# Optimization experiments

Measured on AMD Instinct MI355X. Metric: run time of the kernel, lower is better.

## Reference

```python
import jax, jax.numpy as jnp
import numpy as np

B, S, D_IN, D_OUT = 2, 2048, 4096, 4096
NUM_HEADS, NUM_KV_GROUPS = 32, 8
HEAD_DIM = D_OUT // NUM_HEADS        # 128
GROUP_SIZE = NUM_HEADS // NUM_KV_GROUPS  # 4
ROPE_BASE = 10000.0


def _rope_tables(seq_len, head_dim, base):
    inv_freq = 1.0 / (base ** (jnp.arange(0, head_dim, 2, dtype=jnp.float32) / head_dim))
    pos = jnp.arange(seq_len, dtype=jnp.float32)
    angles = pos[:, None] * inv_freq[None, :]          # (S, hd/2)
    angles = jnp.concatenate([angles, angles], axis=-1)  # (S, hd)
    return jnp.cos(angles), jnp.sin(angles)


def _apply_rope(x, cos, sin):
    # x: (B, H, S, hd)
    hd = x.shape[-1]
    x1, x2 = x[..., : hd // 2], x[..., hd // 2 :]
    rotated = jnp.concatenate([-x2, x1], axis=-1)
    return x * cos[None, None, :, :] + rotated * sin[None, None, :, :]


def setup_inputs() -> dict:
    key = jax.random.key(0)
    k1, k2, k3, k4, k5 = jax.random.split(key, 5)
    s = 0.02
    return {
        "x": jax.random.normal(k1, (B, S, D_IN), jnp.float32),
        "Wq": jax.random.normal(k2, (D_OUT, D_IN), jnp.float32) * s,
        "Wk": jax.random.normal(k3, (NUM_KV_GROUPS * HEAD_DIM, D_IN), jnp.float32) * s,
        "Wv": jax.random.normal(k4, (NUM_KV_GROUPS * HEAD_DIM, D_IN), jnp.float32) * s,
        "Wo": jax.random.normal(k5, (D_OUT, D_OUT), jnp.float32) * s,
    }


def reference(x, Wq, Wk, Wv, Wo):
    b, s, _ = x.shape
    cos, sin = _rope_tables(s, HEAD_DIM, ROPE_BASE)

    # Projections (torch Linear: y = x @ W.T), reshape to (B, H, S, hd)
    q = (x @ Wq.T).reshape(b, s, NUM_HEADS, HEAD_DIM).transpose(0, 2, 1, 3)
    k = (x @ Wk.T).reshape(b, s, NUM_KV_GROUPS, HEAD_DIM).transpose(0, 2, 1, 3)
    v = (x @ Wv.T).reshape(b, s, NUM_KV_GROUPS, HEAD_DIM).transpose(0, 2, 1, 3)

    q = _apply_rope(q, cos, sin)
    k = _apply_rope(k, cos, sin)

    # repeat_interleave KV heads to match query heads
    k = jnp.repeat(k, GROUP_SIZE, axis=1)
    v = jnp.repeat(v, GROUP_SIZE, axis=1)

    scores = jnp.einsum("bhqd,bhkd->bhqk", q, k) / jnp.sqrt(jnp.float32(HEAD_DIM))
    causal = jnp.tril(jnp.ones((s, s), dtype=bool))
    scores = jnp.where(causal[None, None], scores, jnp.finfo(scores.dtype).min)
    attn = jax.nn.softmax(scores, axis=-1)

    ctx = jnp.einsum("bhqk,bhkd->bhqd", attn, v)  # (B, H, S, hd)
    ctx = ctx.transpose(0, 2, 1, 3).reshape(b, s, D_OUT)
    return ctx @ Wo.T
```

## Files before the change

### kernel.cpp

```cpp
#include <hip/hip_runtime.h>


typedef float f32x4 __attribute__((ext_vector_type(4)));
typedef short s16x8 __attribute__((ext_vector_type(8)));

union U8 { s16x8 v; unsigned int u[4]; };

__device__ __forceinline__ unsigned short f32_to_bf16(float f) {
    unsigned int u = __float_as_uint(f);
    u += 0x7fffu + ((u >> 16) & 1u);
    return (unsigned short)(u >> 16);
}
__device__ __forceinline__ float bf16_to_f32(unsigned short h) {
    return __uint_as_float(((unsigned int)h) << 16);
}
__device__ __forceinline__ unsigned int cvt_pk_bf16(float a, float b) {
    unsigned int r;
    asm("v_cvt_pk_bf16_f32 %0, %1, %2" : "=v"(r) : "v"(a), "v"(b));
    return r;
}
__device__ __forceinline__ void async16(const unsigned short* g, unsigned short* l) {
    __builtin_amdgcn_global_load_lds(
        (const __attribute__((address_space(1))) unsigned int*)g,
        (__attribute__((address_space(3))) unsigned int*)l, 16, 0, 0);
}

__global__ __launch_bounds__(256) void cast_f32_bf16(
    const float* __restrict__ in, unsigned short* __restrict__ out, int n4)
{
    int idx = blockIdx.x * 256 + threadIdx.x;
    if (idx >= n4) return;
    float4 v = ((const float4*)in)[idx];
    ushort4 o;
    o.x = f32_to_bf16(v.x); o.y = f32_to_bf16(v.y);
    o.z = f32_to_bf16(v.z); o.w = f32_to_bf16(v.w);
    ((ushort4*)out)[idx] = o;
}

template<int WRITE_F32>
__global__ __launch_bounds__(256) void gemm_bt(
    const unsigned short* __restrict__ A,
    const unsigned short* __restrict__ B,
    void* __restrict__ Cout, int M, int N, int K)
{
    __shared__ __attribute__((aligned(16))) unsigned short sA[2][128*32];
    __shared__ __attribute__((aligned(16))) unsigned short sB[2][128*32];
    const int tid  = threadIdx.x;
    const int lane = tid & 63;
    const int wv   = tid >> 6;
    const int wm   = (wv >> 1) * 64;
    const int wn   = (wv & 1) * 64;
    const int quad = lane >> 4;
    const int lr   = lane & 15;
    const int m0 = blockIdx.y * 128;
    const int n0 = blockIdx.x * 128;

    auto stage = [&](int kt, int bi) {
        const int k0 = kt << 5;
        #pragma unroll
        for (int p = 0; p < 2; ++p) {
            int e  = (p*256 + tid) * 8;
            int r  = e >> 5;
            int cc = (e & 31) >> 3;
            int gc = (cc ^ ((r >> 1) & 3)) * 8;
            async16(&A[(size_t)(m0 + r)*K + k0 + gc], &sA[bi][e]);
            async16(&B[(size_t)(n0 + r)*K + k0 + gc], &sB[bi][e]);
        }
    };

    f32x4 acc[4][4] = {};
    const int nkt = K >> 5;
    stage(0, 0);
    for (int kt = 0; kt < nkt; ++kt) {
        const int buf = kt & 1;
        __syncthreads();
        if (kt + 1 < nkt) stage(kt + 1, buf ^ 1);
        s16x8 af[4], bf[4];
        #pragma unroll
        for (int i = 0; i < 4; ++i) {
            int row = wm + i*16 + lr;
            af[i] = *(const s16x8*)&sA[buf][row*32 + ((quad ^ ((row >> 1) & 3)) * 8)];
        }
        #pragma unroll
        for (int j = 0; j < 4; ++j) {
            int row = wn + j*16 + lr;
            bf[j] = *(const s16x8*)&sB[buf][row*32 + ((quad ^ ((row >> 1) & 3)) * 8)];
        }
        #pragma unroll
        for (int i = 0; i < 4; ++i)
            #pragma unroll
            for (int j = 0; j < 4; ++j)
                acc[i][j] = __builtin_amdgcn_mfma_f32_16x16x32_bf16(af[i], bf[j], acc[i][j], 0, 0, 0);
    }
    #pragma unroll
    for (int i = 0; i < 4; ++i) {
        #pragma unroll
        for (int j = 0; j < 4; ++j) {
            #pragma unroll
            for (int r = 0; r < 4; ++r) {
                size_t row = (size_t)(m0 + wm + i*16 + quad*4 + r);
                size_t col = (size_t)(n0 + wn + j*16 + lr);
                float v = acc[i][j][r];
                if (WRITE_F32) ((float*)Cout)[row*(size_t)N + col] = v;
                else ((unsigned short*)Cout)[row*(size_t)N + col] = f32_to_bf16(v);
            }
        }
    }
}

template<int NHEADS>
__global__ __launch_bounds__(256) void rope_rearrange(
    const unsigned short* __restrict__ in, unsigned short* __restrict__ out,
    int rowstride, float oscale)
{
    constexpr int LH = (NHEADS == 32) ? 5 : 3;
    int idx = blockIdx.x * 256 + threadIdx.x;
    int i  = idx & 63;
    int hh = (idx >> 6) & (NHEADS - 1);
    int s  = (idx >> (6 + LH)) & 2047;
    int b  = idx >> (17 + LH);
    size_t inoff = (size_t)(b*2048 + s) * rowstride + hh*128 + i;
    float x1 = bf16_to_f32(in[inoff]);
    float x2 = bf16_to_f32(in[inoff + 64]);
    float freq = expf((float)i * -0.14391156831212787f);
    float ang  = (float)s * freq;
    float sn, cs;
    sincosf(ang, &sn, &cs);
    size_t outoff = ((size_t)(b*NHEADS + hh) * 2048 + s) * 128 + i;
    out[outoff]      = f32_to_bf16((x1*cs - x2*sn) * oscale);
    out[outoff + 64] = f32_to_bf16((x2*cs + x1*sn) * oscale);
}

__global__ __launch_bounds__(256) void rearrange_vt(
    const unsigned short* __restrict__ in, unsigned short* __restrict__ out)
{
    __shared__ __attribute__((aligned(16))) unsigned short sS[128*136];
    const int tid = threadIdx.x;
    const int bg  = blockIdx.y;
    const int b   = bg >> 3, g = bg & 7;
    const int s0  = blockIdx.x * 128;
    #pragma unroll
    for (int p = 0; p < 8; ++p) {
        int ce = p*256 + tid;
        int s  = ce >> 4, dc = ce & 15;
        s16x8 v = *(const s16x8*)&in[(size_t)(b*2048 + s0 + s)*2048 + 1024 + g*128 + dc*8];
        *(s16x8*)&sS[s*136 + dc*8] = v;
    }
    __syncthreads();
    const int d    = tid & 127;
    const int half = tid >> 7;
    const size_t obase = ((size_t)(bg)*128 + d)*2048 + s0;
    #pragma unroll
    for (int i = 0; i < 8; ++i) {
        int sc   = half*8 + i;
        int blk  = sc >> 3;
        int base = (sc & 7) * 8;
        s16x8 ov;
        #pragma unroll
        for (int j = 0; j < 8; ++j) {
            int p = base + j;
            int soff = blk*64 + ((p >> 5) << 5) + (((p >> 2) & 1) << 4)
                     + (((p >> 3) & 3) << 2) + (p & 3);
            ov[j] = (short)sS[soff*136 + d];
        }
        *(s16x8*)&out[obase + sc*8] = ov;
    }
}

__global__ __launch_bounds__(256, 2) void flash_attn(
    const unsigned short* __restrict__ Q,
    const unsigned short* __restrict__ K,
    const unsigned short* __restrict__ Vt,
    unsigned short* __restrict__ ctx)
{
    __shared__ __attribute__((aligned(16))) unsigned short sK[2][64*128];
    __shared__ __attribute__((aligned(16))) unsigned short sVt[2][128*64];

    const int tid  = threadIdx.x;
    const int lane = tid & 63;
    const int w    = tid >> 6;
    const int quad = lane >> 4;
    const int lr   = lane & 15;
    const int qbi = 15 - blockIdx.x;
    const int b  = blockIdx.y >> 5;
    const int h  = blockIdx.y & 31;
    const int g  = h >> 2;
    const int q0 = qbi * 128;
    const int qw0 = q0 + w * 32;
    const int KT = 2*qbi + 2;

    s16x8 qf[2][4];
    #pragma unroll
    for (int qt = 0; qt < 2; ++qt) {
        const size_t qrow = ((size_t)(b*32 + h) * 2048 + qw0 + qt*16 + lr) * 128;
        #pragma unroll
        for (int kc = 0; kc < 4; ++kc)
            qf[qt][kc] = *(const s16x8*)&Q[qrow + kc*32 + quad*8];
    }
    const size_t kvbase = (size_t)(b*8 + g) * 2048 * 128;
    const size_t vtbase = (size_t)(b*8 + g) * 128 * 2048;

    auto stage = [&](int kt, int bi) {
        const size_t kbase = kvbase + (size_t)kt*64*128;
        #pragma unroll
        for (int p = 0; p < 4; ++p) {
            int e = (p*256 + tid) * 8;
            int r = e >> 7;
            int s = (e & 127) >> 3;
            int gsrc = (s ^ (r & 15)) * 8;
            async16(&K[kbase + (size_t)r*128 + gsrc], &sK[bi][e]);
        }
        #pragma unroll
        for (int p = 0; p < 4; ++p) {
            int ce = p*256 + tid;
            int d  = ce >> 3;
            int c  = ce & 7;
            int gc = (c ^ (d & 7)) * 8;
            async16(&Vt[vtbase + (size_t)d*2048 + kt*64 + gc], &sVt[bi][ce*8]);
        }
    };

    float m_[2] = {-1e30f, -1e30f};
    float l_[2] = {0.f, 0.f};
    f32x4 o[2][8] = {};

    stage(0, 0);
    int buf = 0;
    for (int kt = 0; kt < KT; ++kt) {
        __syncthreads();
        if (kt + 1 < KT) stage(kt + 1, buf ^ 1);

        const bool act = (kt*64 <= qw0 + 31);
        const bool v0  = (kt*64 <= qw0 + 15);
        if (act) {
            f32x4 sacc[2][4] = {};
            __builtin_amdgcn_s_setprio(1);
            #pragma unroll
            for (int ct = 0; ct < 4; ++ct) {
                int row = ct*16 + lr;
                #pragma unroll
                for (int kc = 0; kc < 4; ++kc) {
                    s16x8 kf = *(const s16x8*)&sK[buf][row*128 + (((kc*4 + quad) ^ lr)*8)];
                    if (v0) sacc[0][ct] = __builtin_amdgcn_mfma_f32_16x16x32_bf16(kf, qf[0][kc], sacc[0][ct], 0, 0, 0);
                    sacc[1][ct] = __builtin_amdgcn_mfma_f32_16x16x32_bf16(kf, qf[1][kc], sacc[1][ct], 0, 0, 0);
                }
            }
            __builtin_amdgcn_s_setprio(0);
            U8 pa[2][2];
            #pragma unroll
            for (int qt = 0; qt < 2; ++qt) {
                if (qt == 0 && !v0) continue;
                const int qbase = qw0 + qt*16;
                const bool anymask = (kt*64 + 63) > qbase;
                const int qg = qbase + lr;
                float p[4][4];
                float vmax = -1e30f;
                #pragma unroll
                for (int ct = 0; ct < 4; ++ct)
                    #pragma unroll
                    for (int r = 0; r < 4; ++r) {
                        float sv = sacc[qt][ct][r];
                        if (anymask) {
                            int kv = kt*64 + ct*16 + quad*4 + r;
                            if (kv > qg) sv = -1e30f;
                        }
                        p[ct][r] = sv;
                        vmax = fmaxf(vmax, sv);
                    }
                vmax = fmaxf(vmax, __shfl_xor(vmax, 16));
                vmax = fmaxf(vmax, __shfl_xor(vmax, 32));
                float mcur;
                if (__any(vmax > m_[qt] + 8.f)) {
                    float mnew = fmaxf(m_[qt], vmax);
                    float alpha = exp2f(m_[qt] - mnew);
                    m_[qt] = mnew;
                    mcur = mnew;
                    l_[qt] *= alpha;
                    f32x4 av;
                    #pragma unroll
                    for (int r = 0; r < 4; ++r)
                        av[r] = __shfl(alpha, quad*4 + r);
                    #pragma unroll
                    for (int t = 0; t < 8; ++t)
                        o[qt][t] = o[qt][t] * av;
                } else {
                    mcur = m_[qt];
                }
                float rs = 0.f;
                #pragma unroll
                for (int ct = 0; ct < 4; ++ct)
                    #pragma unroll
                    for (int r = 0; r < 4; ++r) {
                        float pv = exp2f(p[ct][r] - mcur);
                        p[ct][r] = pv;
                        rs += pv;
                    }
                l_[qt] += rs;
                pa[qt][0].u[0] = cvt_pk_bf16(p[0][0], p[0][1]);
                pa[qt][0].u[1] = cvt_pk_bf16(p[0][2], p[0][3]);
                pa[qt][0].u[2] = cvt_pk_bf16(p[1][0], p[1][1]);
                pa[qt][0].u[3] = cvt_pk_bf16(p[1][2], p[1][3]);
                pa[qt][1].u[0] = cvt_pk_bf16(p[2][0], p[2][1]);
                pa[qt][1].u[1] = cvt_pk_bf16(p[2][2], p[2][3]);
                pa[qt][1].u[2] = cvt_pk_bf16(p[3][0], p[3][1]);
                pa[qt][1].u[3] = cvt_pk_bf16(p[3][2], p[3][3]);
            }
            const int dk = lr & 7;
            __builtin_amdgcn_s_setprio(1);
            #pragma unroll
            for (int t = 0; t < 8; ++t) {
                const int d = t*16 + lr;
                #pragma unroll
                for (int c = 0; c < 2; ++c) {
                    s16x8 v8 = *(const s16x8*)&sVt[buf][d*64 + (((c*4 + quad) ^ dk)*8)];
                    if (v0) o[0][t] = __builtin_amdgcn_mfma_f32_16x16x32_bf16(pa[0][c].v, v8, o[0][t], 0, 0, 0);
                    o[1][t] = __builtin_amdgcn_mfma_f32_16x16x32_bf16(pa[1][c].v, v8, o[1][t], 0, 0, 0);
                }
            }
            __builtin_amdgcn_s_setprio(0);
        }
        buf ^= 1;
    }
    #pragma unroll
    for (int qt = 0; qt < 2; ++qt) {
        float lt = l_[qt];
        lt += __shfl_xor(lt, 16);
        lt += __shfl_xor(lt, 32);
        f32x4 lv;
        #pragma unroll
        for (int r = 0; r < 4; ++r)
            lv[r] = __shfl(lt, quad*4 + r);
        #pragma unroll
        for (int r = 0; r < 4; ++r) {
            float inv = 1.0f / lv[r];
            int q = q0 + w*32 + qt*16 + quad*4 + r;
            size_t obase = ((size_t)b*2048 + q) * 4096 + h*128;
            #pragma unroll
            for (int t = 0; t < 8; ++t)
                ctx[obase + t*16 + lr] = f32_to_bf16(o[qt][t][r] * inv);
        }
    }
}

extern "C" void kernel_launch(void* const* d_in, const int* in_sizes, int n_in,
                              void* d_out, int out_size, void* d_ws, size_t ws_size,
                              hipStream_t stream)
{
    const float* x  = (const float*)d_in[0];
    const float* Wq = (const float*)d_in[1];
    const float* Wk = (const float*)d_in[2];
    const float* Wv = (const float*)d_in[3];
    const float* Wo = (const float*)d_in[4];
    float* out = (float*)d_out;
    char* ws = (char*)d_ws;

    unsigned short* xb    = (unsigned short*)(ws);
    unsigned short* Wqb   = (unsigned short*)(ws + 33554432);
    unsigned short* Wkvb  = (unsigned short*)(ws + 67108864);
    unsigned short* Wob   = (unsigned short*)(ws + 83886080);
    unsigned short* Qlin  = (unsigned short*)(ws + 117440512);
    unsigned short* KVlin = (unsigned short*)(ws + 150994944);
    unsigned short* Kr    = (unsigned short*)(ws + 167772160);
    unsigned short* Vt    = (unsigned short*)(ws + 176160768);
    unsigned short* Qr    = xb;
    unsigned short* ctxb  = Qlin;

    cast_f32_bf16<<<16384, 256, 0, stream>>>(x,  xb,  4194304);
    cast_f32_bf16<<<16384, 256, 0, stream>>>(Wq, Wqb, 4194304);
    cast_f32_bf16<<<4096,  256, 0, stream>>>(Wk, Wkvb,           1048576);
    cast_f32_bf16<<<4096,  256, 0, stream>>>(Wv, Wkvb + 4194304, 1048576);
    cast_f32_bf16<<<16384, 256, 0, stream>>>(Wo, Wob, 4194304);

    gemm_bt<0><<<dim3(32, 32), 256, 0, stream>>>(xb, Wqb,  Qlin,  4096, 4096, 4096);
    gemm_bt<0><<<dim3(16, 32), 256, 0, stream>>>(xb, Wkvb, KVlin, 4096, 2048, 4096);

    rope_rearrange<32><<<32768, 256, 0, stream>>>(Qlin,  Qr, 4096, 0.12751646f);
    rope_rearrange<8><<<8192,   256, 0, stream>>>(KVlin, Kr, 2048, 1.0f);
    rearrange_vt<<<dim3(16, 16), 256, 0, stream>>>(KVlin, Vt);

    flash_attn<<<dim3(16, 64), 256, 0, stream>>>(Qr, Kr, Vt, ctxb);

    gemm_bt<1><<<dim3(32, 32), 256, 0, stream>>>(ctxb, Wob, out, 4096, 4096, 4096);
}
```

Baseline: 914.6 us.

## Single-buffer V tile and split the loop into K and V phases with explicit waits

The flash attention loop now double-buffers only K, while V uses a single shared buffer. Each V tile is loaded at the start of its own iteration so the load overlaps the QK^T MFMAs and the softmax. A second barrier with a partial vmcnt wait sits before the PV stage. This halves the V shared memory, which may raise occupancy, at the cost of an extra barrier per iteration and less lookahead for the V loads.

New measurement: 909.7 us. Within noise of the previous version (-0.5%).

```diff
diff --git a/kernel.cpp b/kernel.cpp
--- a/kernel.cpp
+++ b/kernel.cpp
@@ -174,7 +174,7 @@
     unsigned short* __restrict__ ctx)
 {
     __shared__ __attribute__((aligned(16))) unsigned short sK[2][64*128];
-    __shared__ __attribute__((aligned(16))) unsigned short sVt[2][128*64];
+    __shared__ __attribute__((aligned(16))) unsigned short sVt[128*64];
 
     const int tid  = threadIdx.x;
     const int lane = tid & 63;
@@ -200,7 +200,7 @@
     const size_t kvbase = (size_t)(b*8 + g) * 2048 * 128;
     const size_t vtbase = (size_t)(b*8 + g) * 128 * 2048;
 
-    auto stage = [&](int kt, int bi) {
+    auto stageK = [&](int kt, int bi) {
         const size_t kbase = kvbase + (size_t)kt*64*128;
         #pragma unroll
         for (int p = 0; p < 4; ++p) {
@@ -210,13 +210,15 @@
             int gsrc = (s ^ (r & 15)) * 8;
             async16(&K[kbase + (size_t)r*128 + gsrc], &sK[bi][e]);
         }
+    };
+    auto stageV = [&](int kt) {
         #pragma unroll
         for (int p = 0; p < 4; ++p) {
             int ce = p*256 + tid;
             int d  = ce >> 3;
             int c  = ce & 7;
             int gc = (c ^ (d & 7)) * 8;
-            async16(&Vt[vtbase + (size_t)d*2048 + kt*64 + gc], &sVt[bi][ce*8]);
+            async16(&Vt[vtbase + (size_t)d*2048 + kt*64 + gc], &sVt[ce*8]);
         }
     };
 
@@ -224,14 +226,20 @@
     float l_[2] = {0.f, 0.f};
     f32x4 o[2][8] = {};
 
-    stage(0, 0);
-    int buf = 0;
+    stageK(0, 0);
     for (int kt = 0; kt < KT; ++kt) {
-        __syncthreads();
-        if (kt + 1 < KT) stage(kt + 1, buf ^ 1);
+        const int buf = kt & 1;
+        asm volatile("s_waitcnt vmcnt(0)" ::: "memory");
+        __builtin_amdgcn_s_barrier();
+        __builtin_amdgcn_sched_barrier(0);
+        stageV(kt);
+        __builtin_amdgcn_sched_barrier(0);
+        if (kt + 1 < KT) stageK(kt + 1, buf ^ 1);
+        __builtin_amdgcn_sched_barrier(0);
 
         const bool act = (kt*64 <= qw0 + 31);
         const bool v0  = (kt*64 <= qw0 + 15);
+        U8 pa[2][2];
         if (act) {
             f32x4 sacc[2][4] = {};
             __builtin_amdgcn_s_setprio(1);
@@ -246,7 +254,6 @@
                 }
             }
             __builtin_amdgcn_s_setprio(0);
-            U8 pa[2][2];
             #pragma unroll
             for (int qt = 0; qt < 2; ++qt) {
                 if (qt == 0 && !v0) continue;
@@ -305,6 +312,12 @@
                 pa[qt][1].u[2] = cvt_pk_bf16(p[3][0], p[3][1]);
                 pa[qt][1].u[3] = cvt_pk_bf16(p[3][2], p[3][3]);
             }
+        }
+        if (kt + 1 < KT) asm volatile("s_waitcnt vmcnt(4)" ::: "memory");
+        else             asm volatile("s_waitcnt vmcnt(0)" ::: "memory");
+        __builtin_amdgcn_s_barrier();
+        __builtin_amdgcn_sched_barrier(0);
+        if (act) {
             const int dk = lr & 7;
             __builtin_amdgcn_s_setprio(1);
             #pragma unroll
@@ -312,14 +325,13 @@
                 const int d = t*16 + lr;
                 #pragma unroll
                 for (int c = 0; c < 2; ++c) {
-                    s16x8 v8 = *(const s16x8*)&sVt[buf][d*64 + (((c*4 + quad) ^ dk)*8)];
+                    s16x8 v8 = *(const s16x8*)&sVt[d*64 + (((c*4 + quad) ^ dk)*8)];
                     if (v0) o[0][t] = __builtin_amdgcn_mfma_f32_16x16x32_bf16(pa[0][c].v, v8, o[0][t], 0, 0, 0);
                     o[1][t] = __builtin_amdgcn_mfma_f32_16x16x32_bf16(pa[1][c].v, v8, o[1][t], 0, 0, 0);
                 }
             }
             __builtin_amdgcn_s_setprio(0);
         }
-        buf ^= 1;
     }
     #pragma unroll
     for (int qt = 0; qt < 2; ++qt) {
```
